# Optimization experiments

Measured on AMD Instinct MI355X. Metric: run time of the kernel, lower is better.

Reference implementation:

```python
import jax, jax.numpy as jnp
import numpy as np

N_NODES = 50000
N_EDGES = 1000000


def _edge_conv(x, src, dst, W, b, n_nodes):
    """PyG EdgeConv: msg = nn(cat([x_i, x_j - x_i])), aggr=max over incoming edges."""
    xi = x[dst]                      # [E, C] target features
    xj = x[src]                      # [E, C] source features
    m = jnp.concatenate([xi, xj - xi], axis=-1)          # [E, 2C]
    m = jax.nn.relu(m @ W + b)                           # [E, C_out]
    out = jax.ops.segment_max(m, dst, num_segments=n_nodes)  # [N, C_out]
    # empty segments produce -inf; PyG fills with 0
    return jnp.where(jnp.isfinite(out), out, 0.0)


def setup_inputs() -> dict:
    key = jax.random.key(0)
    ks = jax.random.split(key, 12)
    x = jax.random.normal(ks[0], (N_NODES, 3), dtype=jnp.float32)
    edge_index = jax.random.randint(ks[1], (2, N_EDGES), 0, N_NODES, dtype=jnp.int64)

    def lin(k, fan_in, fan_out):
        s = 1.0 / np.sqrt(fan_in)
        kw, kb = jax.random.split(k)
        W = jax.random.uniform(kw, (fan_in, fan_out), jnp.float32, -s, s)
        b = jax.random.uniform(kb, (fan_out,), jnp.float32, -s, s)
        return W, b

    W1, b1 = lin(ks[2], 6, 64)       # conv1 MLP([3*2, 64])
    W2, b2 = lin(ks[3], 128, 128)    # conv2 MLP([64*2, 128])
    W3, b3 = lin(ks[4], 256, 512)    # conv3 MLP([128*2, 512])
    W4, b4 = lin(ks[5], 512, 256)    # lin1 MLP([512, 256])
    W5, b5 = lin(ks[6], 256, 3)      # lin1 final Linear(256, 3)
    return {"x": x, "edge_index": edge_index,
            "W1": W1, "b1": b1, "W2": W2, "b2": b2, "W3": W3, "b3": b3,
            "W4": W4, "b4": b4, "W5": W5, "b5": b5}


def reference(x, edge_index, W1, b1, W2, b2, W3, b3, W4, b4, W5, b5):
    src = edge_index[0]  # x_j
    dst = edge_index[1]  # x_i (aggregation target)
    n = x.shape[0]
    x1 = _edge_conv(x, src, dst, W1, b1, n)    # [N, 64]
    x2 = _edge_conv(x1, src, dst, W2, b2, n)   # [N, 128]
    x3 = _edge_conv(x2, src, dst, W3, b3, n)   # [N, 512]
    x4 = jax.nn.relu(x3 @ W4 + b4) @ W5 + b5   # [N, 3]
    return x + x4
```

## Files before the change

kernel.cpp:

```cpp
#include <hip/hip_runtime.h>

static constexpr int NN = 50000;
static constexpr int NE = 1000000;

typedef short bf16x8 __attribute__((ext_vector_type(8)));
typedef float f32x4 __attribute__((ext_vector_type(4)));

__device__ inline float bf2f_raw(unsigned short u) {
    return __uint_as_float(((unsigned int)u) << 16);
}
__device__ inline unsigned short f2bf(float f) {
    unsigned int u = __float_as_uint(f);
    u += 0x7fffu + ((u >> 16) & 1u);
    return (unsigned short)(u >> 16);
}
__device__ inline void fmax2(float& a0, float& a1, unsigned int v) {
    a0 = fmaxf(a0, bf2f_raw((unsigned short)(v & 0xffffu)));
    a1 = fmaxf(a1, bf2f_raw((unsigned short)(v >> 16)));
}
__device__ inline unsigned int pack2(float f0, float f1) {
    return (unsigned int)f2bf(f0) | ((unsigned int)f2bf(f1) << 16);
}
__device__ inline unsigned int addrelu2(unsigned int a, float t0, float t1) {
    float f0 = fmaxf(bf2f_raw((unsigned short)(a & 0xffffu)) + t0, 0.f);
    float f1 = fmaxf(bf2f_raw((unsigned short)(a >> 16)) + t1, 0.f);
    return pack2(f0, f1);
}


__global__ void setup_kernel(const float* __restrict__ x, const float* __restrict__ W1,
                             const float* __restrict__ b1, const float* __restrict__ b5,
                             const float* __restrict__ W2, const float* __restrict__ W3,
                             const float* __restrict__ W4,
                             unsigned short* __restrict__ as1, float* __restrict__ out,
                             int* __restrict__ deg, int* __restrict__ cursor,
                             unsigned short* __restrict__ Bt2,
                             unsigned short* __restrict__ Bt3,
                             unsigned short* __restrict__ W4t) {
    int t = blockIdx.x * blockDim.x + threadIdx.x;
    if (t < NN * 128) {
        int i = t >> 7, c = t & 127;
        float x0 = x[i * 3 + 0], x1 = x[i * 3 + 1], x2 = x[i * 3 + 2];
        float v;
        if (c < 64) {
            v = x0 * (W1[c] - W1[192 + c]) + x1 * (W1[64 + c] - W1[256 + c]) +
                x2 * (W1[128 + c] - W1[320 + c]) + b1[c];
        } else {
            int cs = c - 64;
            v = x0 * W1[192 + cs] + x1 * W1[256 + cs] + x2 * W1[320 + cs];
        }
        as1[t] = f2bf(v);
        return;
    }
    t -= NN * 128;
    if (t < NN * 3) { out[t] = x[t] + b5[t % 3]; return; }
    t -= NN * 3;
    if (t < NN) { deg[t] = 0; return; }
    t -= NN;
    if (t < NN) { cursor[t] = 0; return; }
    t -= NN;
    if (t < 8192) {
        int k = t / 128, c = t % 128;
        float wt = W2[k * 128 + c];
        float wb = W2[(64 + k) * 128 + c];
        Bt2[c * 64 + k] = f2bf(wt - wb);
        Bt2[(128 + c) * 64 + k] = f2bf(wb);
        return;
    }
    t -= 8192;
    if (t < 65536) {
        int k = t / 512, c = t % 512;
        float wt = W3[k * 512 + c];
        float wb = W3[(128 + k) * 512 + c];
        Bt3[c * 128 + k] = f2bf(wt - wb);
        Bt3[(512 + c) * 128 + k] = f2bf(wb);
        return;
    }
    t -= 65536;
    if (t < 131072) {
        int k = t / 256, n = t % 256;
        W4t[n * 512 + k] = f2bf(W4[k * 256 + n]);
    }
}


__global__ void hist_kernel(const int* __restrict__ dst, int* __restrict__ deg) {
    int e = blockIdx.x * blockDim.x + threadIdx.x;
    if (e < NE) atomicAdd(&deg[dst[e]], 1);
}

__global__ __launch_bounds__(1024) void scan_kernel(const int* __restrict__ deg,
                                                    int* __restrict__ rowstart) {
    __shared__ int wave_sums[16];
    constexpr int CH = (NN + 1023) / 1024;
    int tid = threadIdx.x;
    int lane = tid & 63;
    int wave = tid >> 6;
    int base = tid * CH;
    int vals[CH];
    int sum = 0;
    #pragma unroll
    for (int i = 0; i < CH; ++i) {
        int idx = base + i;
        vals[i] = (idx < NN) ? deg[idx] : 0;
        sum += vals[i];
    }
    int x = sum;
    #pragma unroll
    for (int off = 1; off < 64; off <<= 1) {
        int y = __shfl_up(x, off);
        if (lane >= off) x += y;
    }
    if (lane == 63) wave_sums[wave] = x;
    __syncthreads();
    if (wave == 0 && lane < 16) {
        int s = wave_sums[lane];
        #pragma unroll
        for (int off = 1; off < 16; off <<= 1) {
            int y = __shfl_up(s, off);
            if (lane >= off) s += y;
        }
        wave_sums[lane] = s;
    }
    __syncthreads();
    int run = (wave ? wave_sums[wave - 1] : 0) + x - sum;
    #pragma unroll
    for (int i = 0; i < CH; ++i) {
        int idx = base + i;
        if (idx < NN) rowstart[idx] = run;
        run += vals[i];
    }
    if (tid == 1023) rowstart[NN] = run;
}

__global__ void scatter_kernel(const int* __restrict__ src, const int* __restrict__ dst,
                               const int* __restrict__ rowstart, int* __restrict__ cursor,
                               int* __restrict__ csr) {
    int e = blockIdx.x * blockDim.x + threadIdx.x;
    if (e < NE) {
        int d = dst[e];
        int pos = atomicAdd(&cursor[d], 1);
        csr[rowstart[d] + pos] = src[e];
    }
}


__global__ __launch_bounds__(256) void edge_fused_conv1_kernel(
    const unsigned short* __restrict__ as, const int* __restrict__ rowstart,
    const int* __restrict__ csr, unsigned short* __restrict__ x1) {
    int wid = (blockIdx.x * 256 + threadIdx.x) >> 6;
    int lane = threadIdx.x & 63;
    if (wid >= NN) return;
    int e0 = __builtin_amdgcn_readfirstlane(rowstart[wid]);
    int e1 = __builtin_amdgcn_readfirstlane(rowstart[wid + 1]);
    int h = lane >> 5, c0 = (lane & 31) * 2;
    float t0 = -INFINITY, t1 = -INFINITY;
    const unsigned short* sb = as + 64 + c0;
    int nedge = e1 - e0;
    for (int base = 0; base < nedge; base += 64) {
        int rem = nedge - base;
        int myj = csr[(lane < rem) ? (e0 + base + lane) : e0];
        int cnt = rem < 64 ? rem : 64;
        int cp = (cnt + 7) & ~7;
        for (int q = 0; q < cp; q += 8) {
            int j0 = __shfl(myj, q + 0 + h);
            int j1 = __shfl(myj, q + 2 + h);
            int j2 = __shfl(myj, q + 4 + h);
            int j3 = __shfl(myj, q + 6 + h);
            unsigned int v0 = *(const unsigned int*)(sb + (size_t)j0 * 128);
            unsigned int v1 = *(const unsigned int*)(sb + (size_t)j1 * 128);
            unsigned int v2 = *(const unsigned int*)(sb + (size_t)j2 * 128);
            unsigned int v3 = *(const unsigned int*)(sb + (size_t)j3 * 128);
            fmax2(t0, t1, v0);
            fmax2(t0, t1, v1);
            fmax2(t0, t1, v2);
            fmax2(t0, t1, v3);
        }
    }
    t0 = fmaxf(t0, __shfl_xor(t0, 32));
    t1 = fmaxf(t1, __shfl_xor(t1, 32));
    if (h == 0) {
        unsigned int av = *(const unsigned int*)(as + (size_t)wid * 128 + c0);
        *(unsigned int*)(x1 + (size_t)wid * 64 + c0) = addrelu2(av, t0, t1);
    }
}


__global__ __launch_bounds__(256) void edge_fused128_kernel(
    const unsigned short* __restrict__ as, const int* __restrict__ rowstart,
    const int* __restrict__ csr, unsigned short* __restrict__ xout) {
    int wid = (blockIdx.x * 256 + threadIdx.x) >> 6;
    int lane = threadIdx.x & 63;
    if (wid >= NN) return;
    int e0 = __builtin_amdgcn_readfirstlane(rowstart[wid]);
    int e1 = __builtin_amdgcn_readfirstlane(rowstart[wid + 1]);
    float t0 = -INFINITY, t1 = -INFINITY;
    const unsigned short* sb = as + 128 + (size_t)lane * 2;
    int nedge = e1 - e0;
    for (int base = 0; base < nedge; base += 64) {
        int rem = nedge - base;
        int myj = csr[(lane < rem) ? (e0 + base + lane) : e0];
        int cnt = rem < 64 ? rem : 64;
        int cp = (cnt + 7) & ~7;
        for (int q = 0; q < cp; q += 8) {
            int j0 = __shfl(myj, q + 0), j1 = __shfl(myj, q + 1);
            int j2 = __shfl(myj, q + 2), j3 = __shfl(myj, q + 3);
            int j4 = __shfl(myj, q + 4), j5 = __shfl(myj, q + 5);
            int j6 = __shfl(myj, q + 6), j7 = __shfl(myj, q + 7);
            unsigned int v0 = *(const unsigned int*)(sb + (size_t)j0 * 256);
            unsigned int v1 = *(const unsigned int*)(sb + (size_t)j1 * 256);
            unsigned int v2 = *(const unsigned int*)(sb + (size_t)j2 * 256);
            unsigned int v3 = *(const unsigned int*)(sb + (size_t)j3 * 256);
            unsigned int v4 = *(const unsigned int*)(sb + (size_t)j4 * 256);
            unsigned int v5 = *(const unsigned int*)(sb + (size_t)j5 * 256);
            unsigned int v6 = *(const unsigned int*)(sb + (size_t)j6 * 256);
            unsigned int v7 = *(const unsigned int*)(sb + (size_t)j7 * 256);
            fmax2(t0, t1, v0); fmax2(t0, t1, v1);
            fmax2(t0, t1, v2); fmax2(t0, t1, v3);
            fmax2(t0, t1, v4); fmax2(t0, t1, v5);
            fmax2(t0, t1, v6); fmax2(t0, t1, v7);
        }
    }
    unsigned int av = *(const unsigned int*)(as + (size_t)wid * 256 + lane * 2);
    *(unsigned int*)(xout + (size_t)wid * 128 + lane * 2) = addrelu2(av, t0, t1);
}


__global__ __launch_bounds__(256) void edge_fused512_kernel(
    const unsigned short* __restrict__ as, const int* __restrict__ rowstart,
    const int* __restrict__ csr, unsigned short* __restrict__ xout) {
    int wid = (blockIdx.x * 256 + threadIdx.x) >> 6;
    int lane = threadIdx.x & 63;
    if (wid >= NN) return;
    int e0 = __builtin_amdgcn_readfirstlane(rowstart[wid]);
    int e1 = __builtin_amdgcn_readfirstlane(rowstart[wid + 1]);
    float acc[8];
    #pragma unroll
    for (int v = 0; v < 8; ++v) acc[v] = -INFINITY;
    const unsigned short* sb = as + 512 + (size_t)lane * 8;
    int nedge = e1 - e0;
    for (int base = 0; base < nedge; base += 64) {
        int rem = nedge - base;
        int myj = csr[(lane < rem) ? (e0 + base + lane) : e0];
        int cnt = rem < 64 ? rem : 64;
        int cp = (cnt + 3) & ~3;
        for (int q = 0; q < cp; q += 4) {
            int j0 = __shfl(myj, q + 0), j1 = __shfl(myj, q + 1);
            int j2 = __shfl(myj, q + 2), j3 = __shfl(myj, q + 3);
            uint4 v0 = *(const uint4*)(sb + (size_t)j0 * 1024);
            uint4 v1 = *(const uint4*)(sb + (size_t)j1 * 1024);
            uint4 v2 = *(const uint4*)(sb + (size_t)j2 * 1024);
            uint4 v3 = *(const uint4*)(sb + (size_t)j3 * 1024);
            fmax2(acc[0], acc[1], v0.x); fmax2(acc[2], acc[3], v0.y);
            fmax2(acc[4], acc[5], v0.z); fmax2(acc[6], acc[7], v0.w);
            fmax2(acc[0], acc[1], v1.x); fmax2(acc[2], acc[3], v1.y);
            fmax2(acc[4], acc[5], v1.z); fmax2(acc[6], acc[7], v1.w);
            fmax2(acc[0], acc[1], v2.x); fmax2(acc[2], acc[3], v2.y);
            fmax2(acc[4], acc[5], v2.z); fmax2(acc[6], acc[7], v2.w);
            fmax2(acc[0], acc[1], v3.x); fmax2(acc[2], acc[3], v3.y);
            fmax2(acc[4], acc[5], v3.z); fmax2(acc[6], acc[7], v3.w);
        }
    }
    uint4 av = *(const uint4*)(as + (size_t)wid * 1024 + lane * 8);
    uint4 o;
    o.x = addrelu2(av.x, acc[0], acc[1]);
    o.y = addrelu2(av.y, acc[2], acc[3]);
    o.z = addrelu2(av.z, acc[4], acc[5]);
    o.w = addrelu2(av.w, acc[6], acc[7]);
    *(uint4*)(xout + (size_t)wid * 512 + lane * 8) = o;
}


template<int K, int NT>
__global__ __launch_bounds__(256) void mfma_gemm_nloop_kernel(
    const unsigned short* __restrict__ A, const unsigned short* __restrict__ Bt,
    const float* __restrict__ bias, int bias_n,
    unsigned short* __restrict__ C, int M) {
    constexpr int KC = K / 32;
    constexpr int N = NT * 128;
    __shared__ __align__(16) unsigned short Asl[KC][128 * 40];
    __shared__ __align__(16) unsigned short Bsl[128 * 40];
    int tid = threadIdx.x;
    int mbase = blockIdx.x * 128;
    int wave = tid >> 6, lane = tid & 63;
    int wm = (wave >> 1) * 64, wn = (wave & 1) * 64;
    int quad = lane >> 4, l16 = lane & 15;

    #pragma unroll
    for (int c = tid; c < KC * 512; c += 256) {
        int kc = c >> 9, rem = c & 511;
        int r = rem >> 2, kk = (rem & 3) * 8;
        uint4 va = make_uint4(0u, 0u, 0u, 0u);
        int gr = mbase + r;
        if (gr < M) va = *(const uint4*)&A[(size_t)gr * K + kc * 32 + kk];
        *(uint4*)&Asl[kc][r * 40 + kk] = va;
    }

    for (int nt = 0; nt < NT; ++nt) {
        int nbase = nt * 128;
        f32x4 acc[4][4] = {};
        for (int kc = 0; kc < KC; ++kc) {
            __syncthreads();
            #pragma unroll
            for (int h = 0; h < 2; ++h) {
                int c = tid + h * 256;
                int r = c >> 2, kk = (c & 3) * 8;
                uint4 vb = *(const uint4*)&Bt[(size_t)(nbase + r) * K + kc * 32 + kk];
                *(uint4*)&Bsl[r * 40 + kk] = vb;
            }
            __syncthreads();
            bf16x8 af[4], bfr[4];
            #pragma unroll
            for (int tt = 0; tt < 4; ++tt) {
                af[tt]  = *(const bf16x8*)&Asl[kc][(wm + tt * 16 + l16) * 40 + quad * 8];
                bfr[tt] = *(const bf16x8*)&Bsl[(wn + tt * 16 + l16) * 40 + quad * 8];
            }
            #pragma unroll
            for (int mt = 0; mt < 4; ++mt)
                #pragma unroll
                for (int ntt = 0; ntt < 4; ++ntt)
                    acc[mt][ntt] = __builtin_amdgcn_mfma_f32_16x16x32_bf16(
                        af[mt], bfr[ntt], acc[mt][ntt], 0, 0, 0);
        }
        #pragma unroll
        for (int mt = 0; mt < 4; ++mt) {
            #pragma unroll
            for (int r = 0; r < 4; ++r) {
                int row = mbase + wm + mt * 16 + quad * 4 + r;
                if (row >= M) continue;
                #pragma unroll
                for (int ntt = 0; ntt < 4; ++ntt) {
                    int col = nbase + wn + ntt * 16 + l16;
                    float v = acc[mt][ntt][r];
                    if (col < bias_n) v += bias[col];
                    C[(size_t)row * N + col] = f2bf(v);
                }
            }
        }
    }
}


__global__ __launch_bounds__(256) void mfma_gemm_w5_kernel(
    const unsigned short* __restrict__ A, const unsigned short* __restrict__ Bt,
    const float* __restrict__ b4, const float* __restrict__ W5,
    float* __restrict__ out, int M, int K) {
    __shared__ __align__(16) unsigned short Asl[128 * 40];
    __shared__ __align__(16) unsigned short Bsl[128 * 40];
    int tid = threadIdx.x;
    int mbase = blockIdx.y * 128, nbase = blockIdx.x * 128;
    int wave = tid >> 6, lane = tid & 63;
    int wm = (wave >> 1) * 64, wn = (wave & 1) * 64;
    int quad = lane >> 4, l16 = lane & 15;
    f32x4 acc[4][4] = {};
    for (int kb = 0; kb < K; kb += 32) {
        #pragma unroll
        for (int h = 0; h < 2; ++h) {
            int c = tid + h * 256;
            int r = c >> 2, kk = (c & 3) * 8;
            uint4 va = make_uint4(0u, 0u, 0u, 0u);
            int gr = mbase + r;
            if (gr < M) va = *(const uint4*)&A[(size_t)gr * K + kb + kk];
            *(uint4*)&Asl[r * 40 + kk] = va;
            uint4 vb = *(const uint4*)&Bt[(size_t)(nbase + r) * K + kb + kk];
            *(uint4*)&Bsl[r * 40 + kk] = vb;
        }
        __syncthreads();
        bf16x8 af[4], bfr[4];
        #pragma unroll
        for (int tt = 0; tt < 4; ++tt) {
            af[tt]  = *(const bf16x8*)&Asl[(wm + tt * 16 + l16) * 40 + quad * 8];
            bfr[tt] = *(const bf16x8*)&Bsl[(wn + tt * 16 + l16) * 40 + quad * 8];
        }
        #pragma unroll
        for (int mt = 0; mt < 4; ++mt)
            #pragma unroll
            for (int nt = 0; nt < 4; ++nt)
                acc[mt][nt] = __builtin_amdgcn_mfma_f32_16x16x32_bf16(
                    af[mt], bfr[nt], acc[mt][nt], 0, 0, 0);
        __syncthreads();
    }
    float w5r[4][3], b4v[4];
    #pragma unroll
    for (int nt = 0; nt < 4; ++nt) {
        int col = nbase + wn + nt * 16 + l16;
        b4v[nt] = b4[col];
        w5r[nt][0] = W5[col * 3 + 0];
        w5r[nt][1] = W5[col * 3 + 1];
        w5r[nt][2] = W5[col * 3 + 2];
    }
    #pragma unroll
    for (int mt = 0; mt < 4; ++mt) {
        #pragma unroll
        for (int r = 0; r < 4; ++r) {
            int row = mbase + wm + mt * 16 + quad * 4 + r;
            float p0 = 0.f, p1 = 0.f, p2 = 0.f;
            #pragma unroll
            for (int nt = 0; nt < 4; ++nt) {
                float h = fmaxf(acc[mt][nt][r] + b4v[nt], 0.f);
                p0 += h * w5r[nt][0];
                p1 += h * w5r[nt][1];
                p2 += h * w5r[nt][2];
            }
            #pragma unroll
            for (int m = 8; m; m >>= 1) {
                p0 += __shfl_xor(p0, m);
                p1 += __shfl_xor(p1, m);
                p2 += __shfl_xor(p2, m);
            }
            if (l16 == 0 && row < M) {
                atomicAdd(&out[row * 3 + 0], p0);
                atomicAdd(&out[row * 3 + 1], p1);
                atomicAdd(&out[row * 3 + 2], p2);
            }
        }
    }
}

__global__ void fallback_copy_kernel(const float* __restrict__ x, float* __restrict__ out) {
    int t = blockIdx.x * blockDim.x + threadIdx.x;
    if (t < NN * 3) out[t] = x[t];
}


extern "C" void kernel_launch(void* const* d_in, const int* in_sizes, int n_in,
                              void* d_out, int out_size, void* d_ws, size_t ws_size,
                              hipStream_t stream) {
    const float* x  = (const float*)d_in[0];
    const int*   ei = (const int*)d_in[1];
    const float* W1 = (const float*)d_in[2];
    const float* b1 = (const float*)d_in[3];
    const float* W2 = (const float*)d_in[4];
    const float* b2 = (const float*)d_in[5];
    const float* W3 = (const float*)d_in[6];
    const float* b3 = (const float*)d_in[7];
    const float* W4 = (const float*)d_in[8];
    const float* b4 = (const float*)d_in[9];
    const float* W5 = (const float*)d_in[10];
    const float* b5 = (const float*)d_in[11];
    float* out = (float*)d_out;

    char* p = (char*)d_ws;
    auto alloc = [&](size_t bytes) -> void* {
        void* r = (void*)p;
        p += (bytes + 255) & ~(size_t)255;
        return r;
    };
    int* deg      = (int*)alloc((size_t)NN * 4);
    int* rowstart = (int*)alloc((size_t)(NN + 1) * 4);
    int* cursor   = (int*)alloc((size_t)NN * 4);
    int* csr      = (int*)alloc((size_t)NE * 4);
    unsigned short* Bt2 = (unsigned short*)alloc(256 * 64 * 2);
    unsigned short* Bt3 = (unsigned short*)alloc(1024 * 128 * 2);
    unsigned short* W4t = (unsigned short*)alloc(256 * 512 * 2);
    unsigned short* x1 = (unsigned short*)alloc((size_t)NN * 64 * 2);
    unsigned short* x2 = (unsigned short*)alloc((size_t)NN * 128 * 2);
    unsigned short* x3 = (unsigned short*)alloc((size_t)NN * 512 * 2);
    unsigned short* as_slab = (unsigned short*)alloc((size_t)NN * 1024 * 2);
    size_t need = (size_t)(p - (char*)d_ws);
    if (ws_size < need) {
        fallback_copy_kernel<<<(NN * 3 + 255) / 256, 256, 0, stream>>>(x, out);
        return;
    }

    const int* src = ei;
    const int* dst = ei + NE;

    constexpr int SETUP_T = NN * 128 + NN * 3 + NN + NN + 8192 + 65536 + 131072;
    setup_kernel<<<(SETUP_T + 255) / 256, 256, 0, stream>>>(
        x, W1, b1, b5, W2, W3, W4, as_slab, out, deg, cursor, Bt2, Bt3, W4t);

    hist_kernel<<<(NE + 255) / 256, 256, 0, stream>>>(dst, deg);
    scan_kernel<<<1, 1024, 0, stream>>>(deg, rowstart);
    scatter_kernel<<<(NE + 255) / 256, 256, 0, stream>>>(src, dst, rowstart, cursor, csr);

    edge_fused_conv1_kernel<<<12500, 256, 0, stream>>>(as_slab, rowstart, csr, x1);

    mfma_gemm_nloop_kernel<64, 2><<<391, 256, 0, stream>>>(
        x1, Bt2, b2, 128, as_slab, NN);
    edge_fused128_kernel<<<12500, 256, 0, stream>>>(as_slab, rowstart, csr, x2);

    mfma_gemm_nloop_kernel<128, 8><<<391, 256, 0, stream>>>(
        x2, Bt3, b3, 512, as_slab, NN);
    edge_fused512_kernel<<<12500, 256, 0, stream>>>(as_slab, rowstart, csr, x3);

    mfma_gemm_w5_kernel<<<dim3(2, 391), 256, 0, stream>>>(
        x3, W4t, b4, W5, out, NN, 512);
}
```

Baseline: 618.5 us.

## Fuse conv3 max-aggregation with final W4/W5 MLP head per 16-node tile

Result: faster. 591.0 us (median of 2 runs) (-4.4%).

```diff
diff --git a/kernel.cpp b/kernel.cpp
--- a/kernel.cpp
+++ b/kernel.cpp
@@ -226,48 +226,100 @@
 }
 
 
-__global__ __launch_bounds__(256) void edge_fused512_kernel(
+__global__ __launch_bounds__(256) void ef512_w5_kernel(
     const unsigned short* __restrict__ as, const int* __restrict__ rowstart,
-    const int* __restrict__ csr, unsigned short* __restrict__ xout) {
-    int wid = (blockIdx.x * 256 + threadIdx.x) >> 6;
-    int lane = threadIdx.x & 63;
-    if (wid >= NN) return;
-    int e0 = __builtin_amdgcn_readfirstlane(rowstart[wid]);
-    int e1 = __builtin_amdgcn_readfirstlane(rowstart[wid + 1]);
-    float acc[8];
-    #pragma unroll
-    for (int v = 0; v < 8; ++v) acc[v] = -INFINITY;
+    const int* __restrict__ csr, const unsigned short* __restrict__ W4t,
+    const float* __restrict__ b4, const float* __restrict__ W5,
+    float* __restrict__ out) {
+    __shared__ __align__(16) unsigned short X[16][520];
+    int wave = threadIdx.x >> 6, lane = threadIdx.x & 63;
+    int tilebase = blockIdx.x * 16;
+
     const unsigned short* sb = as + 512 + (size_t)lane * 8;
-    int nedge = e1 - e0;
-    for (int base = 0; base < nedge; base += 64) {
-        int rem = nedge - base;
-        int myj = csr[(lane < rem) ? (e0 + base + lane) : e0];
-        int cnt = rem < 64 ? rem : 64;
-        int cp = (cnt + 3) & ~3;
-        for (int q = 0; q < cp; q += 4) {
-            int j0 = __shfl(myj, q + 0), j1 = __shfl(myj, q + 1);
-            int j2 = __shfl(myj, q + 2), j3 = __shfl(myj, q + 3);
-            uint4 v0 = *(const uint4*)(sb + (size_t)j0 * 1024);
-            uint4 v1 = *(const uint4*)(sb + (size_t)j1 * 1024);
-            uint4 v2 = *(const uint4*)(sb + (size_t)j2 * 1024);
-            uint4 v3 = *(const uint4*)(sb + (size_t)j3 * 1024);
-            fmax2(acc[0], acc[1], v0.x); fmax2(acc[2], acc[3], v0.y);
-            fmax2(acc[4], acc[5], v0.z); fmax2(acc[6], acc[7], v0.w);
-            fmax2(acc[0], acc[1], v1.x); fmax2(acc[2], acc[3], v1.y);
-            fmax2(acc[4], acc[5], v1.z); fmax2(acc[6], acc[7], v1.w);
-            fmax2(acc[0], acc[1], v2.x); fmax2(acc[2], acc[3], v2.y);
-            fmax2(acc[4], acc[5], v2.z); fmax2(acc[6], acc[7], v2.w);
-            fmax2(acc[0], acc[1], v3.x); fmax2(acc[2], acc[3], v3.y);
-            fmax2(acc[4], acc[5], v3.z); fmax2(acc[6], acc[7], v3.w);
-        }
-    }
-    uint4 av = *(const uint4*)(as + (size_t)wid * 1024 + lane * 8);
-    uint4 o;
-    o.x = addrelu2(av.x, acc[0], acc[1]);
-    o.y = addrelu2(av.y, acc[2], acc[3]);
-    o.z = addrelu2(av.z, acc[4], acc[5]);
-    o.w = addrelu2(av.w, acc[6], acc[7]);
-    *(uint4*)(xout + (size_t)wid * 512 + lane * 8) = o;
+    for (int i = 0; i < 4; ++i) {
+        int node = tilebase + wave * 4 + i;
+        int e0 = __builtin_amdgcn_readfirstlane(rowstart[node]);
+        int e1 = __builtin_amdgcn_readfirstlane(rowstart[node + 1]);
+        float acc[8];
+        #pragma unroll
+        for (int v = 0; v < 8; ++v) acc[v] = -INFINITY;
+        int nedge = e1 - e0;
+        for (int base = 0; base < nedge; base += 64) {
+            int rem = nedge - base;
+            int myj = csr[(lane < rem) ? (e0 + base + lane) : e0];
+            int cnt = rem < 64 ? rem : 64;
+            int cp = (cnt + 3) & ~3;
+            for (int q = 0; q < cp; q += 4) {
+                int j0 = __shfl(myj, q + 0), j1 = __shfl(myj, q + 1);
+                int j2 = __shfl(myj, q + 2), j3 = __shfl(myj, q + 3);
+                uint4 v0 = *(const uint4*)(sb + (size_t)j0 * 1024);
+                uint4 v1 = *(const uint4*)(sb + (size_t)j1 * 1024);
+                uint4 v2 = *(const uint4*)(sb + (size_t)j2 * 1024);
+                uint4 v3 = *(const uint4*)(sb + (size_t)j3 * 1024);
+                fmax2(acc[0], acc[1], v0.x); fmax2(acc[2], acc[3], v0.y);
+                fmax2(acc[4], acc[5], v0.z); fmax2(acc[6], acc[7], v0.w);
+                fmax2(acc[0], acc[1], v1.x); fmax2(acc[2], acc[3], v1.y);
+                fmax2(acc[4], acc[5], v1.z); fmax2(acc[6], acc[7], v1.w);
+                fmax2(acc[0], acc[1], v2.x); fmax2(acc[2], acc[3], v2.y);
+                fmax2(acc[4], acc[5], v2.z); fmax2(acc[6], acc[7], v2.w);
+                fmax2(acc[0], acc[1], v3.x); fmax2(acc[2], acc[3], v3.y);
+                fmax2(acc[4], acc[5], v3.z); fmax2(acc[6], acc[7], v3.w);
+            }
+        }
+        uint4 av = *(const uint4*)(as + (size_t)node * 1024 + lane * 8);
+        uint4 o;
+        o.x = addrelu2(av.x, acc[0], acc[1]);
+        o.y = addrelu2(av.y, acc[2], acc[3]);
+        o.z = addrelu2(av.z, acc[4], acc[5]);
+        o.w = addrelu2(av.w, acc[6], acc[7]);
+        *(uint4*)&X[wave * 4 + i][lane * 8] = o;
+    }
+    __syncthreads();
+
+    int quad = lane >> 4, l16 = lane & 15;
+    int colbase = wave * 64;
+    f32x4 acc4[4] = {};
+    for (int kc = 0; kc < 16; ++kc) {
+        bf16x8 afr = *(const bf16x8*)&X[l16][kc * 32 + quad * 8];
+        #pragma unroll
+        for (int nt = 0; nt < 4; ++nt) {
+            int col = colbase + nt * 16 + l16;
+            bf16x8 bfr = *(const bf16x8*)&W4t[(size_t)col * 512 + kc * 32 + quad * 8];
+            acc4[nt] = __builtin_amdgcn_mfma_f32_16x16x32_bf16(afr, bfr, acc4[nt], 0, 0, 0);
+        }
+    }
+    float b4v[4], w5r[4][3];
+    #pragma unroll
+    for (int nt = 0; nt < 4; ++nt) {
+        int col = colbase + nt * 16 + l16;
+        b4v[nt] = b4[col];
+        w5r[nt][0] = W5[col * 3 + 0];
+        w5r[nt][1] = W5[col * 3 + 1];
+        w5r[nt][2] = W5[col * 3 + 2];
+    }
+    #pragma unroll
+    for (int r = 0; r < 4; ++r) {
+        int row = tilebase + quad * 4 + r;
+        float p0 = 0.f, p1 = 0.f, p2 = 0.f;
+        #pragma unroll
+        for (int nt = 0; nt < 4; ++nt) {
+            float h = fmaxf(acc4[nt][r] + b4v[nt], 0.f);
+            p0 += h * w5r[nt][0];
+            p1 += h * w5r[nt][1];
+            p2 += h * w5r[nt][2];
+        }
+        #pragma unroll
+        for (int m = 8; m; m >>= 1) {
+            p0 += __shfl_xor(p0, m);
+            p1 += __shfl_xor(p1, m);
+            p2 += __shfl_xor(p2, m);
+        }
+        if (l16 == 0) {
+            atomicAdd(&out[row * 3 + 0], p0);
+            atomicAdd(&out[row * 3 + 1], p1);
+            atomicAdd(&out[row * 3 + 2], p2);
+        }
+    }
 }
 
 
@@ -340,83 +392,6 @@
     }
 }
 
-
-__global__ __launch_bounds__(256) void mfma_gemm_w5_kernel(
-    const unsigned short* __restrict__ A, const unsigned short* __restrict__ Bt,
-    const float* __restrict__ b4, const float* __restrict__ W5,
-    float* __restrict__ out, int M, int K) {
-    __shared__ __align__(16) unsigned short Asl[128 * 40];
-    __shared__ __align__(16) unsigned short Bsl[128 * 40];
-    int tid = threadIdx.x;
-    int mbase = blockIdx.y * 128, nbase = blockIdx.x * 128;
-    int wave = tid >> 6, lane = tid & 63;
-    int wm = (wave >> 1) * 64, wn = (wave & 1) * 64;
-    int quad = lane >> 4, l16 = lane & 15;
-    f32x4 acc[4][4] = {};
-    for (int kb = 0; kb < K; kb += 32) {
-        #pragma unroll
-        for (int h = 0; h < 2; ++h) {
-            int c = tid + h * 256;
-            int r = c >> 2, kk = (c & 3) * 8;
-            uint4 va = make_uint4(0u, 0u, 0u, 0u);
-            int gr = mbase + r;
-            if (gr < M) va = *(const uint4*)&A[(size_t)gr * K + kb + kk];
-            *(uint4*)&Asl[r * 40 + kk] = va;
-            uint4 vb = *(const uint4*)&Bt[(size_t)(nbase + r) * K + kb + kk];
-            *(uint4*)&Bsl[r * 40 + kk] = vb;
-        }
-        __syncthreads();
-        bf16x8 af[4], bfr[4];
-        #pragma unroll
-        for (int tt = 0; tt < 4; ++tt) {
-            af[tt]  = *(const bf16x8*)&Asl[(wm + tt * 16 + l16) * 40 + quad * 8];
-            bfr[tt] = *(const bf16x8*)&Bsl[(wn + tt * 16 + l16) * 40 + quad * 8];
-        }
-        #pragma unroll
-        for (int mt = 0; mt < 4; ++mt)
-            #pragma unroll
-            for (int nt = 0; nt < 4; ++nt)
-                acc[mt][nt] = __builtin_amdgcn_mfma_f32_16x16x32_bf16(
-                    af[mt], bfr[nt], acc[mt][nt], 0, 0, 0);
-        __syncthreads();
-    }
-    float w5r[4][3], b4v[4];
-    #pragma unroll
-    for (int nt = 0; nt < 4; ++nt) {
-        int col = nbase + wn + nt * 16 + l16;
-        b4v[nt] = b4[col];
-        w5r[nt][0] = W5[col * 3 + 0];
-        w5r[nt][1] = W5[col * 3 + 1];
-        w5r[nt][2] = W5[col * 3 + 2];
-    }
-    #pragma unroll
-    for (int mt = 0; mt < 4; ++mt) {
-        #pragma unroll
-        for (int r = 0; r < 4; ++r) {
-            int row = mbase + wm + mt * 16 + quad * 4 + r;
-            float p0 = 0.f, p1 = 0.f, p2 = 0.f;
-            #pragma unroll
-            for (int nt = 0; nt < 4; ++nt) {
-                float h = fmaxf(acc[mt][nt][r] + b4v[nt], 0.f);
-                p0 += h * w5r[nt][0];
-                p1 += h * w5r[nt][1];
-                p2 += h * w5r[nt][2];
-            }
-            #pragma unroll
-            for (int m = 8; m; m >>= 1) {
-                p0 += __shfl_xor(p0, m);
-                p1 += __shfl_xor(p1, m);
-                p2 += __shfl_xor(p2, m);
-            }
-            if (l16 == 0 && row < M) {
-                atomicAdd(&out[row * 3 + 0], p0);
-                atomicAdd(&out[row * 3 + 1], p1);
-                atomicAdd(&out[row * 3 + 2], p2);
-            }
-        }
-    }
-}
-
 __global__ void fallback_copy_kernel(const float* __restrict__ x, float* __restrict__ out) {
     int t = blockIdx.x * blockDim.x + threadIdx.x;
     if (t < NN * 3) out[t] = x[t];
@@ -455,7 +430,6 @@
     unsigned short* W4t = (unsigned short*)alloc(256 * 512 * 2);
     unsigned short* x1 = (unsigned short*)alloc((size_t)NN * 64 * 2);
     unsigned short* x2 = (unsigned short*)alloc((size_t)NN * 128 * 2);
-    unsigned short* x3 = (unsigned short*)alloc((size_t)NN * 512 * 2);
     unsigned short* as_slab = (unsigned short*)alloc((size_t)NN * 1024 * 2);
     size_t need = (size_t)(p - (char*)d_ws);
     if (ws_size < need) {
@@ -482,8 +456,7 @@
 
     mfma_gemm_nloop_kernel<128, 8><<<391, 256, 0, stream>>>(
         x2, Bt3, b3, 512, as_slab, NN);
-    edge_fused512_kernel<<<12500, 256, 0, stream>>>(as_slab, rowstart, csr, x3);
-
-    mfma_gemm_w5_kernel<<<dim3(2, 391), 256, 0, stream>>>(
-        x3, W4t, b4, W5, out, NN, 512);
-}
+
+    ef512_w5_kernel<<<NN / 16, 256, 0, stream>>>(
+        as_slab, rowstart, csr, W4t, b4, W5, out);
+}
```
